# Kernel tuning notes

Measured on AMD Instinct MI355X. Metric: run time of the kernel, lower is better.

The kernel has to match this reference:

```python
import jax, jax.numpy as jnp
import numpy as np

N = 50000      # nodes
E = 1600000    # edges (avg degree 32)
C_IN = 128
C_H = 128
C_OUT = 10
G = 512        # number of graphs in the batch


def setup_inputs() -> dict:
    key = jax.random.key(0)
    ks = jax.random.split(key, 16)
    x = jax.random.normal(ks[0], (N, C_IN), dtype=jnp.float32)
    edge_index = jax.random.randint(ks[1], (2, E), 0, N, dtype=jnp.int64)
    batch = jnp.sort(jax.random.randint(ks[2], (N,), 0, G, dtype=jnp.int64))

    def lin(k, fan_in, fan_out):
        lim = 1.0 / np.sqrt(fan_in)
        return jax.random.uniform(k, (fan_in, fan_out), jnp.float32, -lim, lim)

    return {
        "x": x, "edge_index": edge_index, "batch": batch,
        # conv1: c_in -> c_hidden
        "Wr1": lin(ks[3], C_IN, C_H), "br1": jnp.zeros((C_H,), jnp.float32),
        "Wo1": lin(ks[4], C_IN, C_H),
        # conv2: c_hidden -> 2*c_hidden
        "Wr2": lin(ks[5], C_H, 2 * C_H), "br2": jnp.zeros((2 * C_H,), jnp.float32),
        "Wo2": lin(ks[6], C_H, 2 * C_H),
        # conv3: 2*c_hidden -> c_hidden
        "Wr3": lin(ks[7], 2 * C_H, C_H), "br3": jnp.zeros((C_H,), jnp.float32),
        "Wo3": lin(ks[8], 2 * C_H, C_H),
        # head
        "W1": lin(ks[9], C_H, 4 * C_OUT), "b1": jnp.zeros((4 * C_OUT,), jnp.float32),
        "W2": lin(ks[10], 4 * C_OUT, C_OUT), "b2": jnp.zeros((C_OUT,), jnp.float32),
    }


def _graph_conv(x, src, dst, Wr, br, Wo):
    # PyG GraphConv: lin_rel(sum_{j in N(i)} x_j) + lin_root(x_i)
    agg = jax.ops.segment_sum(x[src], dst, num_segments=N)  # [N, F_in]
    return agg @ Wr + br + x @ Wo


def reference(x, edge_index, batch, Wr1, br1, Wo1, Wr2, br2, Wo2,
              Wr3, br3, Wo3, W1, b1, W2, b2):
    src, dst = edge_index[0], edge_index[1]
    h = jax.nn.relu(_graph_conv(x, src, dst, Wr1, br1, Wo1))
    h = jax.nn.relu(_graph_conv(h, src, dst, Wr2, br2, Wo2))
    h = _graph_conv(h, src, dst, Wr3, br3, Wo3)
    # global mean pool over graphs
    sums = jax.ops.segment_sum(h, batch, num_segments=G)            # [G, C_H]
    cnts = jax.ops.segment_sum(jnp.ones((N,), h.dtype), batch, num_segments=G)
    pooled = sums / jnp.maximum(cnts, 1.0)[:, None]
    # dropout is identity in eval mode
    out = pooled @ W1 + b1
    out = out @ W2 + b2
    return out
```

## Files before the change

kernel.cpp:

```cpp
#include <hip/hip_runtime.h>
#include <hip/hip_bf16.h>
#include <cstddef>

#define NN 50000
#define EE 1600000
#define GG 512
#define NB 196
#define BSTRIDE 16384
#define BCAP 10240
#define XBLKS 6250
#define SCBLKS 782

typedef unsigned int u32;
typedef unsigned short u16;
typedef __attribute__((ext_vector_type(8))) short frag_ab;
typedef __attribute__((ext_vector_type(4))) float frag_cd;

__device__ __forceinline__ void gl_lds16(const void* g, void* l) {
    __builtin_amdgcn_global_load_lds(
        (const __attribute__((address_space(1))) u32*)g,
        (__attribute__((address_space(3))) u32*)l, 16, 0, 0);
}
__device__ __forceinline__ float b2f_lo(u32 v) { return __uint_as_float(v << 16); }
__device__ __forceinline__ float b2f_hi(u32 v) { return __uint_as_float(v & 0xffff0000u); }
__device__ __forceinline__ float b2f(u32 v, int odd) { return odd ? b2f_hi(v) : b2f_lo(v); }
__device__ __forceinline__ u16 f2b(float x) {
    __hip_bfloat16 h = __float2bfloat16(x);
    return *(u16*)&h;
}
__device__ __forceinline__ u32 pack2(float lo, float hi) {
    return ((u32)f2b(hi) << 16) | f2b(lo);
}
__device__ __forceinline__ void acc2(float2& a, u32 v) {
    a.x += b2f_lo(v);
    a.y += b2f_hi(v);
}


__global__ __launch_bounds__(256) void bscatter_prep_kernel(
    const int* __restrict__ ei, int* __restrict__ bcnt, u32* __restrict__ pairs,
    const float* __restrict__ x, u16* __restrict__ ax,
    const float* __restrict__ Wr1, const float* __restrict__ Wo1,
    const float* __restrict__ Wr2, const float* __restrict__ Wo2,
    const float* __restrict__ Wr3, const float* __restrict__ Wo3,
    const float* __restrict__ br3,
    u16* __restrict__ BT1, u16* __restrict__ BT2, u16* __restrict__ BT3,
    float* __restrict__ bias3) {
    __shared__ int lcnt[NB];
    __shared__ int lbase[NB];
    __shared__ unsigned short lpos[2048];
    int bid = blockIdx.x, t = threadIdx.x;
    if (bid < SCBLKS) {
        int e0 = bid * 2048;
        u32 pk[8];
        int bk[8];
        for (int i = t; i < NB; i += 256) lcnt[i] = 0;
        __syncthreads();
#pragma unroll
        for (int i = 0; i < 8; ++i) {
            int e = e0 + i * 256 + t;
            if (e < EE) {
                int dst = ei[EE + e], src = ei[e];
                int b = dst >> 8;
                bk[i] = b;
                pk[i] = ((u32)src << 8) | (u32)(dst & 255);
                lpos[i * 256 + t] = (unsigned short)atomicAdd(&lcnt[b], 1);
            } else bk[i] = -1;
        }
        __syncthreads();
        for (int i = t; i < NB; i += 256) lbase[i] = atomicAdd(&bcnt[i], lcnt[i]);
        __syncthreads();
#pragma unroll
        for (int i = 0; i < 8; ++i) {
            if (bk[i] >= 0) {
                int pos = lbase[bk[i]] + (int)lpos[i * 256 + t];
                pairs[(size_t)bk[i] * BSTRIDE + pos] = pk[i];
            }
        }
    } else if (bid < SCBLKS + XBLKS) {
        int idx = (bid - SCBLKS) * 256 + t;
        int row = idx >> 5, q = idx & 31;
        float4 v = *(const float4*)(x + (size_t)row * 128 + q * 4);
        *(u32*)(ax + (size_t)row * 256 + 128 + q * 4) = pack2(v.x, v.y);
        *(u32*)(ax + (size_t)row * 256 + 128 + q * 4 + 2) = pack2(v.z, v.w);
    } else {
        int m = bid - SCBLKS - XBLKS;
        int k = t;
        BT2[m * 256 + k] = f2b(k < 128 ? Wr2[k * 256 + m] : Wo2[(k - 128) * 256 + m]);
        BT3[m * 256 + k] = f2b(m < 128 ? Wr3[k * 128 + m] : Wo3[k * 128 + (m - 128)]);
        if (m < 128)
            BT1[m * 256 + k] = f2b(k < 128 ? Wr1[k * 128 + m] : Wo1[(k - 128) * 128 + m]);
        if (k == 0) bias3[m] = (m < 128) ? 0.f : br3[m - 128];
    }
}


__global__ __launch_bounds__(512) void bfill_kernel(const u32* __restrict__ pairs,
                                                    const int* __restrict__ bcnt,
                                                    int* __restrict__ ofs,
                                                    u16* __restrict__ srcl) {
    __shared__ int sc[256];
    __shared__ int cnts[256];
    __shared__ int lcnt[256];
    __shared__ int lcur[256];
    __shared__ int lbuf[BCAP];
    int b = blockIdx.x, t = threadIdx.x;
    if (t < 256) {
        int c = (t < NB) ? bcnt[t] : 0;
        cnts[t] = c;
        sc[t] = c;
        lcnt[t] = 0;
    }
    __syncthreads();
    for (int off = 1; off < 256; off <<= 1) {
        int v = (t >= off && t < 256) ? sc[t - off] : 0;
        __syncthreads();
        if (t < 256) sc[t] += v;
        __syncthreads();
    }
    int base = sc[b] - cnts[b];
    int span = cnts[b];
    const u32* pp = pairs + (size_t)b * BSTRIDE;
    for (int j = t; j < span; j += 512) atomicAdd(&lcnt[pp[j] & 255u], 1);
    __syncthreads();
    int nc = 0;
    if (t < 256) {
        nc = lcnt[t];
        sc[t] = nc;
    }
    __syncthreads();
    for (int off = 1; off < 256; off <<= 1) {
        int v = (t >= off && t < 256) ? sc[t - off] : 0;
        __syncthreads();
        if (t < 256) sc[t] += v;
        __syncthreads();
    }
    if (t < 256) {
        int excl = sc[t] - nc;
        int node = b * 256 + t;
        if (node < NN) ofs[node] = base + excl;
        lcur[t] = excl;
    }
    if (b == 0 && t == 256) ofs[NN] = EE;
    __syncthreads();
    for (int j = t; j < span; j += 512) {
        u32 p = pp[j];
        int pos = atomicAdd(&lcur[p & 255u], 1);
        int src = (int)(p >> 8);
        if (pos < BCAP) lbuf[pos] = src;
        else srcl[base + pos] = (u16)src;
    }
    __syncthreads();
    int lim = span < BCAP ? span : BCAP;
    for (int j = t; j < lim; j += 512) srcl[base + j] = (u16)lbuf[j];
}


__global__ __launch_bounds__(256) void pull_bf_kernel(const u32* __restrict__ Xu,
                                                      const int* __restrict__ ofs,
                                                      const u16* __restrict__ srcl,
                                                      u32* __restrict__ outu) {
    int node = (blockIdx.x * 256 + threadIdx.x) >> 6;
    int lane = threadIdx.x & 63;
    int q = lane >> 4, l = lane & 15;
    int lo = ofs[node], hi = ofs[node + 1];
    float2 a0 = {0.f, 0.f}, a1 = {0.f, 0.f}, a2 = {0.f, 0.f}, a3 = {0.f, 0.f};
    int j = lo;
    for (; j + 15 < hi; j += 16) {
        int s0 = srcl[j + q], s1 = srcl[j + 4 + q];
        int s2 = srcl[j + 8 + q], s3 = srcl[j + 12 + q];
        uint4 v0 = *(const uint4*)(Xu + (size_t)s0 * 128 + l * 4);
        uint4 v1 = *(const uint4*)(Xu + (size_t)s1 * 128 + l * 4);
        uint4 v2 = *(const uint4*)(Xu + (size_t)s2 * 128 + l * 4);
        uint4 v3 = *(const uint4*)(Xu + (size_t)s3 * 128 + l * 4);
        acc2(a0, v0.x); acc2(a1, v0.y); acc2(a2, v0.z); acc2(a3, v0.w);
        acc2(a0, v1.x); acc2(a1, v1.y); acc2(a2, v1.z); acc2(a3, v1.w);
        acc2(a0, v2.x); acc2(a1, v2.y); acc2(a2, v2.z); acc2(a3, v2.w);
        acc2(a0, v3.x); acc2(a1, v3.y); acc2(a2, v3.z); acc2(a3, v3.w);
    }
    for (; j + 3 < hi; j += 4) {
        int s = srcl[j + q];
        uint4 v = *(const uint4*)(Xu + (size_t)s * 128 + l * 4);
        acc2(a0, v.x); acc2(a1, v.y); acc2(a2, v.z); acc2(a3, v.w);
    }
    if (j + q < hi) {
        int s = srcl[j + q];
        uint4 v = *(const uint4*)(Xu + (size_t)s * 128 + l * 4);
        acc2(a0, v.x); acc2(a1, v.y); acc2(a2, v.z); acc2(a3, v.w);
    }
    float acc[8] = {a0.x, a0.y, a1.x, a1.y, a2.x, a2.y, a3.x, a3.y};
#pragma unroll
    for (int i = 0; i < 8; ++i) {
        acc[i] += __shfl_xor(acc[i], 16, 64);
        acc[i] += __shfl_xor(acc[i], 32, 64);
    }
    if (q == 0) {
        uint4 r;
        r.x = pack2(acc[0], acc[1]);
        r.y = pack2(acc[2], acc[3]);
        r.z = pack2(acc[4], acc[5]);
        r.w = pack2(acc[6], acc[7]);
        *(uint4*)(outu + (size_t)node * 128 + l * 4) = r;
    }
}

__global__ __launch_bounds__(256) void pull3_kernel(const u32* __restrict__ Tu,
                                                    const int* __restrict__ ofs,
                                                    const u16* __restrict__ srcl,
                                                    u32* __restrict__ h3u) {
    int node = (blockIdx.x * 256 + threadIdx.x) >> 6;
    int lane = threadIdx.x & 63;
    int q = lane >> 4, l = lane & 15;
    int lo = ofs[node], hi = ofs[node + 1];
    float2 a0 = {0.f, 0.f}, a1 = {0.f, 0.f}, a2 = {0.f, 0.f}, a3 = {0.f, 0.f};
    int j = lo;
    for (; j + 15 < hi; j += 16) {
        int s0 = srcl[j + q], s1 = srcl[j + 4 + q];
        int s2 = srcl[j + 8 + q], s3 = srcl[j + 12 + q];
        uint4 v0 = *(const uint4*)(Tu + (size_t)s0 * 128 + l * 4);
        uint4 v1 = *(const uint4*)(Tu + (size_t)s1 * 128 + l * 4);
        uint4 v2 = *(const uint4*)(Tu + (size_t)s2 * 128 + l * 4);
        uint4 v3 = *(const uint4*)(Tu + (size_t)s3 * 128 + l * 4);
        acc2(a0, v0.x); acc2(a1, v0.y); acc2(a2, v0.z); acc2(a3, v0.w);
        acc2(a0, v1.x); acc2(a1, v1.y); acc2(a2, v1.z); acc2(a3, v1.w);
        acc2(a0, v2.x); acc2(a1, v2.y); acc2(a2, v2.z); acc2(a3, v2.w);
        acc2(a0, v3.x); acc2(a1, v3.y); acc2(a2, v3.z); acc2(a3, v3.w);
    }
    for (; j + 3 < hi; j += 4) {
        int s = srcl[j + q];
        uint4 v = *(const uint4*)(Tu + (size_t)s * 128 + l * 4);
        acc2(a0, v.x); acc2(a1, v.y); acc2(a2, v.z); acc2(a3, v.w);
    }
    if (j + q < hi) {
        int s = srcl[j + q];
        uint4 v = *(const uint4*)(Tu + (size_t)s * 128 + l * 4);
        acc2(a0, v.x); acc2(a1, v.y); acc2(a2, v.z); acc2(a3, v.w);
    }
    float acc[8] = {a0.x, a0.y, a1.x, a1.y, a2.x, a2.y, a3.x, a3.y};
#pragma unroll
    for (int i = 0; i < 8; ++i) {
        acc[i] += __shfl_xor(acc[i], 16, 64);
        acc[i] += __shfl_xor(acc[i], 32, 64);
    }
    if (q == 0) {
        uint4 o = *(const uint4*)(Tu + (size_t)node * 128 + 64 + l * 4);
        acc[0] += b2f_lo(o.x); acc[1] += b2f_hi(o.x);
        acc[2] += b2f_lo(o.y); acc[3] += b2f_hi(o.y);
        acc[4] += b2f_lo(o.z); acc[5] += b2f_hi(o.z);
        acc[6] += b2f_lo(o.w); acc[7] += b2f_hi(o.w);
        uint4 r;
        r.x = pack2(acc[0], acc[1]);
        r.y = pack2(acc[2], acc[3]);
        r.z = pack2(acc[4], acc[5]);
        r.w = pack2(acc[6], acc[7]);
        *(uint4*)(h3u + (size_t)node * 64 + l * 4) = r;
    }
}


__global__ __launch_bounds__(256, 2) void gemm_bf_kernel(
    const u16* __restrict__ A, const u16* __restrict__ BT,
    const float* __restrict__ bias, u16* __restrict__ C,
    int ldc, int coloff, int relu) {
    __shared__ alignas(16) u16 As[128 * 32];
    __shared__ alignas(16) u16 Bs[128 * 32];
    const int t = threadIdx.x;
    const int lane = t & 63, wid = t >> 6;
    const int quad = lane >> 4, l16 = lane & 15;
    const int wm = wid >> 1, wn = wid & 1;
    const int row0 = blockIdx.y * 128, c0 = blockIdx.x * 128;

    frag_cd acc[4][4];
#pragma unroll
    for (int i = 0; i < 4; ++i)
#pragma unroll
        for (int j = 0; j < 4; ++j) acc[i][j] = (frag_cd)0.f;

    const int ca = t, cb = t + 256;
    const int ra = ca >> 2, oa = (ca & 3) * 8;
    const int rb = cb >> 2, ob = (cb & 3) * 8;
    const int garow = min(row0 + ra, NN - 1);
    const int gbrow = min(row0 + rb, NN - 1);
    const size_t gA1 = (size_t)garow * 256 + oa;
    const size_t gA2 = (size_t)gbrow * 256 + ob;
    const size_t gB1 = (size_t)(c0 + ra) * 256 + oa;
    const size_t gB2 = (size_t)(c0 + rb) * 256 + ob;

    for (int kk = 0; kk < 256; kk += 32) {
        __syncthreads();
        gl_lds16(A + gA1 + kk, &As[ca * 8]);
        gl_lds16(A + gA2 + kk, &As[cb * 8]);
        gl_lds16(BT + gB1 + kk, &Bs[ca * 8]);
        gl_lds16(BT + gB2 + kk, &Bs[cb * 8]);
        __syncthreads();

        frag_ab a[4], b[4];
#pragma unroll
        for (int mt = 0; mt < 4; ++mt)
            a[mt] = *(const frag_ab*)&As[(wm * 64 + mt * 16 + l16) * 32 + quad * 8];
#pragma unroll
        for (int nt = 0; nt < 4; ++nt)
            b[nt] = *(const frag_ab*)&Bs[(wn * 64 + nt * 16 + l16) * 32 + quad * 8];
#pragma unroll
        for (int mt = 0; mt < 4; ++mt)
#pragma unroll
            for (int nt = 0; nt < 4; ++nt)
                acc[mt][nt] = __builtin_amdgcn_mfma_f32_16x16x32_bf16(
                    a[mt], b[nt], acc[mt][nt], 0, 0, 0);
    }

#pragma unroll
    for (int nt = 0; nt < 4; ++nt) {
        int col = c0 + wn * 64 + nt * 16 + l16;
        float bv = bias[col];
#pragma unroll
        for (int mt = 0; mt < 4; ++mt) {
#pragma unroll
            for (int r = 0; r < 4; ++r) {
                int row = row0 + wm * 64 + mt * 16 + quad * 4 + r;
                if (row < NN) {
                    float v = acc[mt][nt][r] + bv;
                    if (relu) v = fmaxf(v, 0.f);
                    C[(size_t)row * ldc + coloff + col] = f2b(v);
                }
            }
        }
    }
}


__device__ inline int lower_bound_i(const int* a, int n, int v) {
    int lo = 0, hi = n;
    while (lo < hi) {
        int m = (lo + hi) >> 1;
        if (a[m] < v) lo = m + 1; else hi = m;
    }
    return lo;
}

__global__ __launch_bounds__(256) void pool_head_kernel(const u32* __restrict__ h3u,
                                                        const int* __restrict__ batch,
                                                        const float* __restrict__ W1,
                                                        const float* __restrict__ b1,
                                                        const float* __restrict__ W2,
                                                        const float* __restrict__ b2,
                                                        float* __restrict__ out) {
    __shared__ float ps[256];
    __shared__ float p[128];
    __shared__ float hid[40];
    int g = blockIdx.x, t = threadIdx.x;
    int c = t & 127, half = t >> 7;
    int w = c >> 1, odd = c & 1;
    int lo = lower_bound_i(batch, NN, g);
    int hi = lower_bound_i(batch, NN, g + 1);
    float s = 0.f;
    int i = lo + half;
    for (; i + 6 < hi; i += 8) {
        u32 v0 = h3u[(size_t)i * 64 + w];
        u32 v1 = h3u[(size_t)(i + 2) * 64 + w];
        u32 v2 = h3u[(size_t)(i + 4) * 64 + w];
        u32 v3 = h3u[(size_t)(i + 6) * 64 + w];
        s += (b2f(v0, odd) + b2f(v1, odd)) + (b2f(v2, odd) + b2f(v3, odd));
    }
    for (; i < hi; i += 2) s += b2f(h3u[(size_t)i * 64 + w], odd);
    ps[t] = s;
    __syncthreads();
    if (half == 0) p[c] = (ps[c] + ps[c + 128]) / fmaxf((float)(hi - lo), 1.f);
    __syncthreads();
    if (t < 40) {
        float v = b1[t];
        for (int k = 0; k < 128; ++k) v += p[k] * W1[k * 40 + t];
        hid[t] = v;
    }
    __syncthreads();
    if (t < 10) {
        float v = b2[t];
        for (int j = 0; j < 40; ++j) v += hid[j] * W2[j * 10 + t];
        out[g * 10 + t] = v;
    }
}


extern "C" void kernel_launch(void* const* d_in, const int* in_sizes, int n_in,
                              void* d_out, int out_size, void* d_ws, size_t ws_size,
                              hipStream_t stream) {
    const float* x   = (const float*)d_in[0];
    const int* ei    = (const int*)d_in[1];
    const int* batch = (const int*)d_in[2];
    const float* Wr1 = (const float*)d_in[3];
    const float* br1 = (const float*)d_in[4];
    const float* Wo1 = (const float*)d_in[5];
    const float* Wr2 = (const float*)d_in[6];
    const float* br2 = (const float*)d_in[7];
    const float* Wo2 = (const float*)d_in[8];
    const float* Wr3 = (const float*)d_in[9];
    const float* br3 = (const float*)d_in[10];
    const float* Wo3 = (const float*)d_in[11];
    const float* W1  = (const float*)d_in[12];
    const float* b1  = (const float*)d_in[13];
    const float* W2  = (const float*)d_in[14];
    const float* b2  = (const float*)d_in[15];
    float* out = (float*)d_out;

    char* ws = (char*)d_ws;
    size_t off = 0;
    auto alloc = [&](size_t bytes) {
        void* p = ws + off;
        off += (bytes + 255) & ~(size_t)255;
        return p;
    };
    int* ofs      = (int*)alloc((NN + 1) * sizeof(int));
    int* bcnt     = (int*)alloc(256 * sizeof(int));
    u16* srcl     = (u16*)alloc((size_t)EE * 2);
    u16* ax       = (u16*)alloc((size_t)NN * 256 * 2);
    u16* ah1      = (u16*)alloc((size_t)NN * 256 * 2);
    u16* h2       = (u16*)alloc((size_t)NN * 256 * 2);
    u16* t3o3     = (u16*)alloc((size_t)NN * 256 * 2);
    u16* h3       = (u16*)alloc((size_t)NN * 128 * 2);
    u16* BT1      = (u16*)alloc(128 * 256 * 2);
    u16* BT2      = (u16*)alloc(256 * 256 * 2);
    u16* BT3      = (u16*)alloc(256 * 256 * 2);
    float* bias3  = (float*)alloc(256 * sizeof(float));
    u32* pairs = (u32*)h2;

    hipMemsetAsync(bcnt, 0, 256 * sizeof(int), stream);

    bscatter_prep_kernel<<<SCBLKS + XBLKS + 256, 256, 0, stream>>>(
        ei, bcnt, pairs, x, ax, Wr1, Wo1, Wr2, Wo2, Wr3, Wo3, br3,
        BT1, BT2, BT3, bias3);
    bfill_kernel<<<NB, 512, 0, stream>>>(pairs, bcnt, ofs, srcl);

    pull_bf_kernel<<<NN * 64 / 256, 256, 0, stream>>>((const u32*)ax + 64, ofs, srcl, (u32*)ax);
    gemm_bf_kernel<<<dim3(1, 391), 256, 0, stream>>>(ax, BT1, br1, ah1, 256, 128, 1);
    pull_bf_kernel<<<NN * 64 / 256, 256, 0, stream>>>((const u32*)ah1 + 64, ofs, srcl, (u32*)ah1);
    gemm_bf_kernel<<<dim3(2, 391), 256, 0, stream>>>(ah1, BT2, br2, h2, 256, 0, 1);
    gemm_bf_kernel<<<dim3(2, 391), 256, 0, stream>>>(h2, BT3, bias3, t3o3, 256, 0, 0);
    pull3_kernel<<<NN * 64 / 256, 256, 0, stream>>>((const u32*)t3o3, ofs, srcl, (u32*)h3);

    pool_head_kernel<<<GG, 256, 0, stream>>>((const u32*)h3, batch, W1, b1, W2, b2, out);
}
```

Baseline: 360.8 us.

## Split gathered features into 32-column slabs for cache-friendly gather passes

Stores the gathered node features in four column-sliced slabs (32 bf16 per row, 64 bytes) instead of 256-wide interleaved rows. Each gather kernel now runs four passes over the grid, one per slab, so each pass's working set is a quarter of the feature matrix and may stay resident in L2/MALL. The GEMM gains modes to read the split layout and write sliced or row-major outputs. The cost is more lanes per edge, extra shuffle reductions, four times more index reads, and less efficient 64-byte gathers.

Result: slower. 472.9 us (+31.1%).

```diff
diff --git a/kernel.cpp b/kernel.cpp
--- a/kernel.cpp
+++ b/kernel.cpp
@@ -37,9 +37,10 @@
 }
 
 
+
 __global__ __launch_bounds__(256) void bscatter_prep_kernel(
     const int* __restrict__ ei, int* __restrict__ bcnt, u32* __restrict__ pairs,
-    const float* __restrict__ x, u16* __restrict__ ax,
+    const float* __restrict__ x, u32* __restrict__ xslu,
     const float* __restrict__ Wr1, const float* __restrict__ Wo1,
     const float* __restrict__ Wr2, const float* __restrict__ Wo2,
     const float* __restrict__ Wr3, const float* __restrict__ Wo3,
@@ -81,8 +82,12 @@
         int idx = (bid - SCBLKS) * 256 + t;
         int row = idx >> 5, q = idx & 31;
         float4 v = *(const float4*)(x + (size_t)row * 128 + q * 4);
-        *(u32*)(ax + (size_t)row * 256 + 128 + q * 4) = pack2(v.x, v.y);
-        *(u32*)(ax + (size_t)row * 256 + 128 + q * 4 + 2) = pack2(v.z, v.w);
+        int s = q >> 3;
+        u32* dst = xslu + (((size_t)(s * NN + row)) << 4) + ((q & 7) << 1);
+        uint2 w;
+        w.x = pack2(v.x, v.y);
+        w.y = pack2(v.z, v.w);
+        *(uint2*)dst = w;
     } else {
         int m = bid - SCBLKS - XBLKS;
         int k = t;
@@ -156,41 +161,40 @@
 }
 
 
-__global__ __launch_bounds__(256) void pull_bf_kernel(const u32* __restrict__ Xu,
+__global__ __launch_bounds__(256) void pull_sl_kernel(const u32* __restrict__ Xsl,
                                                       const int* __restrict__ ofs,
                                                       const u16* __restrict__ srcl,
-                                                      u32* __restrict__ outu) {
-    int node = (blockIdx.x * 256 + threadIdx.x) >> 6;
+                                                      u32* __restrict__ aggu) {
+    int node = blockIdx.x * 4 + (threadIdx.x >> 6);
+    int p = blockIdx.y;
     int lane = threadIdx.x & 63;
-    int q = lane >> 4, l = lane & 15;
+    int q = lane >> 2, l = lane & 3;
+    const u32* base = Xsl + ((size_t)p * NN << 4);
     int lo = ofs[node], hi = ofs[node + 1];
     float2 a0 = {0.f, 0.f}, a1 = {0.f, 0.f}, a2 = {0.f, 0.f}, a3 = {0.f, 0.f};
     int j = lo;
-    for (; j + 15 < hi; j += 16) {
-        int s0 = srcl[j + q], s1 = srcl[j + 4 + q];
-        int s2 = srcl[j + 8 + q], s3 = srcl[j + 12 + q];
-        uint4 v0 = *(const uint4*)(Xu + (size_t)s0 * 128 + l * 4);
-        uint4 v1 = *(const uint4*)(Xu + (size_t)s1 * 128 + l * 4);
-        uint4 v2 = *(const uint4*)(Xu + (size_t)s2 * 128 + l * 4);
-        uint4 v3 = *(const uint4*)(Xu + (size_t)s3 * 128 + l * 4);
+    for (; j + 31 < hi; j += 32) {
+        int s0 = srcl[j + q], s1 = srcl[j + 16 + q];
+        uint4 v0 = *(const uint4*)(base + ((size_t)s0 << 4) + l * 4);
+        uint4 v1 = *(const uint4*)(base + ((size_t)s1 << 4) + l * 4);
         acc2(a0, v0.x); acc2(a1, v0.y); acc2(a2, v0.z); acc2(a3, v0.w);
         acc2(a0, v1.x); acc2(a1, v1.y); acc2(a2, v1.z); acc2(a3, v1.w);
-        acc2(a0, v2.x); acc2(a1, v2.y); acc2(a2, v2.z); acc2(a3, v2.w);
-        acc2(a0, v3.x); acc2(a1, v3.y); acc2(a2, v3.z); acc2(a3, v3.w);
-    }
-    for (; j + 3 < hi; j += 4) {
+    }
+    for (; j + 15 < hi; j += 16) {
         int s = srcl[j + q];
-        uint4 v = *(const uint4*)(Xu + (size_t)s * 128 + l * 4);
+        uint4 v = *(const uint4*)(base + ((size_t)s << 4) + l * 4);
         acc2(a0, v.x); acc2(a1, v.y); acc2(a2, v.z); acc2(a3, v.w);
     }
     if (j + q < hi) {
         int s = srcl[j + q];
-        uint4 v = *(const uint4*)(Xu + (size_t)s * 128 + l * 4);
+        uint4 v = *(const uint4*)(base + ((size_t)s << 4) + l * 4);
         acc2(a0, v.x); acc2(a1, v.y); acc2(a2, v.z); acc2(a3, v.w);
     }
     float acc[8] = {a0.x, a0.y, a1.x, a1.y, a2.x, a2.y, a3.x, a3.y};
 #pragma unroll
     for (int i = 0; i < 8; ++i) {
+        acc[i] += __shfl_xor(acc[i], 4, 64);
+        acc[i] += __shfl_xor(acc[i], 8, 64);
         acc[i] += __shfl_xor(acc[i], 16, 64);
         acc[i] += __shfl_xor(acc[i], 32, 64);
     }
@@ -200,50 +204,50 @@
         r.y = pack2(acc[2], acc[3]);
         r.z = pack2(acc[4], acc[5]);
         r.w = pack2(acc[6], acc[7]);
-        *(uint4*)(outu + (size_t)node * 128 + l * 4) = r;
-    }
-}
-
-__global__ __launch_bounds__(256) void pull3_kernel(const u32* __restrict__ Tu,
-                                                    const int* __restrict__ ofs,
-                                                    const u16* __restrict__ srcl,
-                                                    u32* __restrict__ h3u) {
-    int node = (blockIdx.x * 256 + threadIdx.x) >> 6;
+        *(uint4*)(aggu + (size_t)node * 64 + p * 16 + l * 4) = r;
+    }
+}
+
+__global__ __launch_bounds__(256) void pull3_sl_kernel(const u32* __restrict__ Tsl,
+                                                       const u32* __restrict__ o3u,
+                                                       const int* __restrict__ ofs,
+                                                       const u16* __restrict__ srcl,
+                                                       u32* __restrict__ h3u) {
+    int node = blockIdx.x * 4 + (threadIdx.x >> 6);
+    int p = blockIdx.y;
     int lane = threadIdx.x & 63;
-    int q = lane >> 4, l = lane & 15;
+    int q = lane >> 2, l = lane & 3;
+    const u32* base = Tsl + ((size_t)p * NN << 4);
     int lo = ofs[node], hi = ofs[node + 1];
     float2 a0 = {0.f, 0.f}, a1 = {0.f, 0.f}, a2 = {0.f, 0.f}, a3 = {0.f, 0.f};
     int j = lo;
-    for (; j + 15 < hi; j += 16) {
-        int s0 = srcl[j + q], s1 = srcl[j + 4 + q];
-        int s2 = srcl[j + 8 + q], s3 = srcl[j + 12 + q];
-        uint4 v0 = *(const uint4*)(Tu + (size_t)s0 * 128 + l * 4);
-        uint4 v1 = *(const uint4*)(Tu + (size_t)s1 * 128 + l * 4);
-        uint4 v2 = *(const uint4*)(Tu + (size_t)s2 * 128 + l * 4);
-        uint4 v3 = *(const uint4*)(Tu + (size_t)s3 * 128 + l * 4);
+    for (; j + 31 < hi; j += 32) {
+        int s0 = srcl[j + q], s1 = srcl[j + 16 + q];
+        uint4 v0 = *(const uint4*)(base + ((size_t)s0 << 4) + l * 4);
+        uint4 v1 = *(const uint4*)(base + ((size_t)s1 << 4) + l * 4);
         acc2(a0, v0.x); acc2(a1, v0.y); acc2(a2, v0.z); acc2(a3, v0.w);
         acc2(a0, v1.x); acc2(a1, v1.y); acc2(a2, v1.z); acc2(a3, v1.w);
-        acc2(a0, v2.x); acc2(a1, v2.y); acc2(a2, v2.z); acc2(a3, v2.w);
-        acc2(a0, v3.x); acc2(a1, v3.y); acc2(a2, v3.z); acc2(a3, v3.w);
-    }
-    for (; j + 3 < hi; j += 4) {
+    }
+    for (; j + 15 < hi; j += 16) {
         int s = srcl[j + q];
-        uint4 v = *(const uint4*)(Tu + (size_t)s * 128 + l * 4);
+        uint4 v = *(const uint4*)(base + ((size_t)s << 4) + l * 4);
         acc2(a0, v.x); acc2(a1, v.y); acc2(a2, v.z); acc2(a3, v.w);
     }
     if (j + q < hi) {
         int s = srcl[j + q];
-        uint4 v = *(const uint4*)(Tu + (size_t)s * 128 + l * 4);
+        uint4 v = *(const uint4*)(base + ((size_t)s << 4) + l * 4);
         acc2(a0, v.x); acc2(a1, v.y); acc2(a2, v.z); acc2(a3, v.w);
     }
     float acc[8] = {a0.x, a0.y, a1.x, a1.y, a2.x, a2.y, a3.x, a3.y};
 #pragma unroll
     for (int i = 0; i < 8; ++i) {
+        acc[i] += __shfl_xor(acc[i], 4, 64);
+        acc[i] += __shfl_xor(acc[i], 8, 64);
         acc[i] += __shfl_xor(acc[i], 16, 64);
         acc[i] += __shfl_xor(acc[i], 32, 64);
     }
     if (q == 0) {
-        uint4 o = *(const uint4*)(Tu + (size_t)node * 128 + 64 + l * 4);
+        uint4 o = *(const uint4*)(o3u + (size_t)node * 64 + p * 16 + l * 4);
         acc[0] += b2f_lo(o.x); acc[1] += b2f_hi(o.x);
         acc[2] += b2f_lo(o.y); acc[3] += b2f_hi(o.y);
         acc[4] += b2f_lo(o.z); acc[5] += b2f_hi(o.z);
@@ -253,15 +257,16 @@
         r.y = pack2(acc[2], acc[3]);
         r.z = pack2(acc[4], acc[5]);
         r.w = pack2(acc[6], acc[7]);
-        *(uint4*)(h3u + (size_t)node * 64 + l * 4) = r;
+        *(uint4*)(h3u + (size_t)node * 64 + p * 16 + l * 4) = r;
     }
 }
 
 
 __global__ __launch_bounds__(256, 2) void gemm_bf_kernel(
-    const u16* __restrict__ A, const u16* __restrict__ BT,
-    const float* __restrict__ bias, u16* __restrict__ C,
-    int ldc, int coloff, int relu) {
+    const u16* __restrict__ A0, const u16* __restrict__ A1,
+    const u16* __restrict__ BT, const float* __restrict__ bias,
+    u16* __restrict__ C0, u16* __restrict__ C1,
+    int amode, int cmode, int relu) {
     __shared__ alignas(16) u16 As[128 * 32];
     __shared__ alignas(16) u16 Bs[128 * 32];
     const int t = threadIdx.x;
@@ -281,17 +286,25 @@
     const int rb = cb >> 2, ob = (cb & 3) * 8;
     const int garow = min(row0 + ra, NN - 1);
     const int gbrow = min(row0 + rb, NN - 1);
-    const size_t gA1 = (size_t)garow * 256 + oa;
-    const size_t gA2 = (size_t)gbrow * 256 + ob;
-    const size_t gB1 = (size_t)(c0 + ra) * 256 + oa;
-    const size_t gB2 = (size_t)(c0 + rb) * 256 + ob;
 
     for (int kk = 0; kk < 256; kk += 32) {
-        __syncthreads();
-        gl_lds16(A + gA1 + kk, &As[ca * 8]);
-        gl_lds16(A + gA2 + kk, &As[cb * 8]);
-        gl_lds16(BT + gB1 + kk, &Bs[ca * 8]);
-        gl_lds16(BT + gB2 + kk, &Bs[cb * 8]);
+        const u16 *pa, *pb;
+        if (amode) {
+            pa = A0 + (size_t)garow * 256 + kk + oa;
+            pb = A0 + (size_t)gbrow * 256 + kk + ob;
+        } else if (kk < 128) {
+            pa = A0 + (size_t)garow * 128 + kk + oa;
+            pb = A0 + (size_t)gbrow * 128 + kk + ob;
+        } else {
+            int s = (kk >> 5) - 4;
+            pa = A1 + (((size_t)(s * NN + garow)) << 5) + oa;
+            pb = A1 + (((size_t)(s * NN + gbrow)) << 5) + ob;
+        }
+        __syncthreads();
+        gl_lds16(pa, &As[ca * 8]);
+        gl_lds16(pb, &As[cb * 8]);
+        gl_lds16(BT + (size_t)(c0 + ra) * 256 + kk + oa, &Bs[ca * 8]);
+        gl_lds16(BT + (size_t)(c0 + rb) * 256 + kk + ob, &Bs[cb * 8]);
         __syncthreads();
 
         frag_ab a[4], b[4];
@@ -311,7 +324,8 @@
 
 #pragma unroll
     for (int nt = 0; nt < 4; ++nt) {
-        int col = c0 + wn * 64 + nt * 16 + l16;
+        int col128 = wn * 64 + nt * 16 + l16;
+        int col = c0 + col128;
         float bv = bias[col];
 #pragma unroll
         for (int mt = 0; mt < 4; ++mt) {
@@ -321,7 +335,17 @@
                 if (row < NN) {
                     float v = acc[mt][nt][r] + bv;
                     if (relu) v = fmaxf(v, 0.f);
-                    C[(size_t)row * ldc + coloff + col] = f2b(v);
+                    u16 hv = f2b(v);
+                    if (cmode == 0) {
+                        C0[(((size_t)((col128 >> 5) * NN + row)) << 5) + (col128 & 31)] = hv;
+                    } else if (cmode == 1) {
+                        C0[(size_t)row * 256 + col] = hv;
+                    } else {
+                        if (col < 128)
+                            C0[(((size_t)((col >> 5) * NN + row)) << 5) + (col & 31)] = hv;
+                        else
+                            C1[(size_t)row * 128 + (col - 128)] = hv;
+                    }
                 }
             }
         }
@@ -412,10 +436,13 @@
     int* ofs      = (int*)alloc((NN + 1) * sizeof(int));
     int* bcnt     = (int*)alloc(256 * sizeof(int));
     u16* srcl     = (u16*)alloc((size_t)EE * 2);
-    u16* ax       = (u16*)alloc((size_t)NN * 256 * 2);
-    u16* ah1      = (u16*)alloc((size_t)NN * 256 * 2);
+    u16* xsl      = (u16*)alloc((size_t)NN * 128 * 2);
+    u16* agg1     = (u16*)alloc((size_t)NN * 128 * 2);
+    u16* h1sl     = (u16*)alloc((size_t)NN * 128 * 2);
+    u16* agg2     = (u16*)alloc((size_t)NN * 128 * 2);
     u16* h2       = (u16*)alloc((size_t)NN * 256 * 2);
-    u16* t3o3     = (u16*)alloc((size_t)NN * 256 * 2);
+    u16* t3sl     = (u16*)alloc((size_t)NN * 128 * 2);
+    u16* o3       = (u16*)alloc((size_t)NN * 128 * 2);
     u16* h3       = (u16*)alloc((size_t)NN * 128 * 2);
     u16* BT1      = (u16*)alloc(128 * 256 * 2);
     u16* BT2      = (u16*)alloc(256 * 256 * 2);
@@ -426,16 +453,22 @@
     hipMemsetAsync(bcnt, 0, 256 * sizeof(int), stream);
 
     bscatter_prep_kernel<<<SCBLKS + XBLKS + 256, 256, 0, stream>>>(
-        ei, bcnt, pairs, x, ax, Wr1, Wo1, Wr2, Wo2, Wr3, Wo3, br3,
+        ei, bcnt, pairs, x, (u32*)xsl, Wr1, Wo1, Wr2, Wo2, Wr3, Wo3, br3,
         BT1, BT2, BT3, bias3);
     bfill_kernel<<<NB, 512, 0, stream>>>(pairs, bcnt, ofs, srcl);
 
-    pull_bf_kernel<<<NN * 64 / 256, 256, 0, stream>>>((const u32*)ax + 64, ofs, srcl, (u32*)ax);
-    gemm_bf_kernel<<<dim3(1, 391), 256, 0, stream>>>(ax, BT1, br1, ah1, 256, 128, 1);
-    pull_bf_kernel<<<NN * 64 / 256, 256, 0, stream>>>((const u32*)ah1 + 64, ofs, srcl, (u32*)ah1);
-    gemm_bf_kernel<<<dim3(2, 391), 256, 0, stream>>>(ah1, BT2, br2, h2, 256, 0, 1);
-    gemm_bf_kernel<<<dim3(2, 391), 256, 0, stream>>>(h2, BT3, bias3, t3o3, 256, 0, 0);
-    pull3_kernel<<<NN * 64 / 256, 256, 0, stream>>>((const u32*)t3o3, ofs, srcl, (u32*)h3);
+    pull_sl_kernel<<<dim3(NN / 4, 4), 256, 0, stream>>>(
+        (const u32*)xsl, ofs, srcl, (u32*)agg1);
+    gemm_bf_kernel<<<dim3(1, 391), 256, 0, stream>>>(
+        agg1, xsl, BT1, br1, h1sl, nullptr, 0, 0, 1);
+    pull_sl_kernel<<<dim3(NN / 4, 4), 256, 0, stream>>>(
+        (const u32*)h1sl, ofs, srcl, (u32*)agg2);
+    gemm_bf_kernel<<<dim3(2, 391), 256, 0, stream>>>(
+        agg2, h1sl, BT2, br2, h2, nullptr, 0, 1, 1);
+    gemm_bf_kernel<<<dim3(2, 391), 256, 0, stream>>>(
+        h2, nullptr, BT3, bias3, t3sl, o3, 1, 2, 0);
+    pull3_sl_kernel<<<dim3(NN / 4, 4), 256, 0, stream>>>(
+        (const u32*)t3sl, (const u32*)o3, ofs, srcl, (u32*)h3);
 
     pool_head_kernel<<<GG, 256, 0, stream>>>((const u32*)h3, batch, W1, b1, W2, b2, out);
 }
```

## Fuse conv2 and conv3 GEMMs keeping hidden tile in LDS

Applied to the files above, without the earlier changes.

Replaces the two back-to-back GEMM launches (conv2 with ReLU, then conv3's combined weights) with one kernel that computes a 128-row tile of h2 into a 64 KB swizzled LDS buffer and feeds it straight into the second GEMM. This removes the global write and re-read of the N×256 bf16 h2 intermediate and one launch. In exchange, each block uses about 80 KB of LDS, which limits occupancy. The grid also shrinks to 391 blocks covering all 256 columns, and the staging loop has no double buffering.

New measurement: 352.5 us. 2.3% less time.

```diff
diff --git a/kernel.cpp b/kernel.cpp
--- a/kernel.cpp
+++ b/kernel.cpp
@@ -35,6 +35,7 @@
     a.x += b2f_lo(v);
     a.y += b2f_hi(v);
 }
+
 
 
 __global__ __launch_bounds__(256) void bscatter_prep_kernel(
@@ -322,6 +323,124 @@
                     float v = acc[mt][nt][r] + bv;
                     if (relu) v = fmaxf(v, 0.f);
                     C[(size_t)row * ldc + coloff + col] = f2b(v);
+                }
+            }
+        }
+    }
+}
+
+
+__global__ __launch_bounds__(256, 2) void gemm23_kernel(
+    const u16* __restrict__ A, const u16* __restrict__ BT2,
+    const float* __restrict__ br2, const u16* __restrict__ BT3,
+    const float* __restrict__ bias3, u16* __restrict__ C) {
+    __shared__ alignas(16) u16 As[128 * 32];
+    __shared__ alignas(16) u16 Bs[128 * 32];
+    __shared__ alignas(16) u16 Hs[128 * 256];
+    const int t = threadIdx.x;
+    const int lane = t & 63, wid = t >> 6;
+    const int quad = lane >> 4, l16 = lane & 15;
+    const int wm = wid >> 1, wn = wid & 1;
+    const int row0 = blockIdx.x * 128;
+
+    const int ca = t, cb = t + 256;
+    const int ra = ca >> 2, oa = (ca & 3) * 8;
+    const int rb = cb >> 2, ob = (cb & 3) * 8;
+    const int garow = min(row0 + ra, NN - 1);
+    const int gbrow = min(row0 + rb, NN - 1);
+    const size_t gA1 = (size_t)garow * 256 + oa;
+    const size_t gA2 = (size_t)gbrow * 256 + ob;
+
+    for (int nb = 0; nb < 2; ++nb) {
+        const int c0 = nb * 128;
+        frag_cd acc[4][4];
+#pragma unroll
+        for (int i = 0; i < 4; ++i)
+#pragma unroll
+            for (int j = 0; j < 4; ++j) acc[i][j] = (frag_cd)0.f;
+
+        for (int kk = 0; kk < 256; kk += 32) {
+            __syncthreads();
+            gl_lds16(A + gA1 + kk, &As[ca * 8]);
+            gl_lds16(A + gA2 + kk, &As[cb * 8]);
+            gl_lds16(BT2 + (size_t)(c0 + ra) * 256 + kk + oa, &Bs[ca * 8]);
+            gl_lds16(BT2 + (size_t)(c0 + rb) * 256 + kk + ob, &Bs[cb * 8]);
+            __syncthreads();
+
+            frag_ab a[4], b[4];
+#pragma unroll
+            for (int mt = 0; mt < 4; ++mt)
+                a[mt] = *(const frag_ab*)&As[(wm * 64 + mt * 16 + l16) * 32 + quad * 8];
+#pragma unroll
+            for (int nt = 0; nt < 4; ++nt)
+                b[nt] = *(const frag_ab*)&Bs[(wn * 64 + nt * 16 + l16) * 32 + quad * 8];
+#pragma unroll
+            for (int mt = 0; mt < 4; ++mt)
+#pragma unroll
+                for (int nt = 0; nt < 4; ++nt)
+                    acc[mt][nt] = __builtin_amdgcn_mfma_f32_16x16x32_bf16(
+                        a[mt], b[nt], acc[mt][nt], 0, 0, 0);
+        }
+#pragma unroll
+        for (int nt = 0; nt < 4; ++nt) {
+            int col = c0 + wn * 64 + nt * 16 + l16;
+            float bv = br2[col];
+#pragma unroll
+            for (int mt = 0; mt < 4; ++mt) {
+#pragma unroll
+                for (int r = 0; r < 4; ++r) {
+                    int lr = wm * 64 + mt * 16 + quad * 4 + r;
+                    float v = fmaxf(acc[mt][nt][r] + bv, 0.f);
+                    Hs[(lr * 256 + col) ^ ((lr & 7) << 3)] = f2b(v);
+                }
+            }
+        }
+    }
+    __syncthreads();
+
+    for (int nb = 0; nb < 2; ++nb) {
+        const int c0 = nb * 128;
+        frag_cd acc[4][4];
+#pragma unroll
+        for (int i = 0; i < 4; ++i)
+#pragma unroll
+            for (int j = 0; j < 4; ++j) acc[i][j] = (frag_cd)0.f;
+
+        for (int kk = 0; kk < 256; kk += 32) {
+            __syncthreads();
+            gl_lds16(BT3 + (size_t)(c0 + ra) * 256 + kk + oa, &Bs[ca * 8]);
+            gl_lds16(BT3 + (size_t)(c0 + rb) * 256 + kk + ob, &Bs[cb * 8]);
+            __syncthreads();
+
+            frag_ab a[4], b[4];
+#pragma unroll
+            for (int mt = 0; mt < 4; ++mt) {
+                int lr = wm * 64 + mt * 16 + l16;
+                a[mt] = *(const frag_ab*)&Hs[(lr * 256 + kk + quad * 8) ^ ((lr & 7) << 3)];
+            }
+#pragma unroll
+            for (int nt = 0; nt < 4; ++nt)
+                b[nt] = *(const frag_ab*)&Bs[(wn * 64 + nt * 16 + l16) * 32 + quad * 8];
+#pragma unroll
+            for (int mt = 0; mt < 4; ++mt)
+#pragma unroll
+                for (int nt = 0; nt < 4; ++nt)
+                    acc[mt][nt] = __builtin_amdgcn_mfma_f32_16x16x32_bf16(
+                        a[mt], b[nt], acc[mt][nt], 0, 0, 0);
+        }
+#pragma unroll
+        for (int nt = 0; nt < 4; ++nt) {
+            int col = c0 + wn * 64 + nt * 16 + l16;
+            float bv = bias3[col];
+#pragma unroll
+            for (int mt = 0; mt < 4; ++mt) {
+#pragma unroll
+                for (int r = 0; r < 4; ++r) {
+                    int row = row0 + wm * 64 + mt * 16 + quad * 4 + r;
+                    if (row < NN) {
+                        float v = acc[mt][nt][r] + bv;
+                        C[(size_t)row * 256 + col] = f2b(v);
+                    }
                 }
             }
         }
@@ -414,14 +533,13 @@
     u16* srcl     = (u16*)alloc((size_t)EE * 2);
     u16* ax       = (u16*)alloc((size_t)NN * 256 * 2);
     u16* ah1      = (u16*)alloc((size_t)NN * 256 * 2);
-    u16* h2       = (u16*)alloc((size_t)NN * 256 * 2);
     u16* t3o3     = (u16*)alloc((size_t)NN * 256 * 2);
     u16* h3       = (u16*)alloc((size_t)NN * 128 * 2);
     u16* BT1      = (u16*)alloc(128 * 256 * 2);
     u16* BT2      = (u16*)alloc(256 * 256 * 2);
     u16* BT3      = (u16*)alloc(256 * 256 * 2);
     float* bias3  = (float*)alloc(256 * sizeof(float));
-    u32* pairs = (u32*)h2;
+    u32* pairs = (u32*)t3o3;
 
     hipMemsetAsync(bcnt, 0, 256 * sizeof(int), stream);
 
@@ -433,8 +551,7 @@
     pull_bf_kernel<<<NN * 64 / 256, 256, 0, stream>>>((const u32*)ax + 64, ofs, srcl, (u32*)ax);
     gemm_bf_kernel<<<dim3(1, 391), 256, 0, stream>>>(ax, BT1, br1, ah1, 256, 128, 1);
     pull_bf_kernel<<<NN * 64 / 256, 256, 0, stream>>>((const u32*)ah1 + 64, ofs, srcl, (u32*)ah1);
-    gemm_bf_kernel<<<dim3(2, 391), 256, 0, stream>>>(ah1, BT2, br2, h2, 256, 0, 1);
-    gemm_bf_kernel<<<dim3(2, 391), 256, 0, stream>>>(h2, BT3, bias3, t3o3, 256, 0, 0);
+    gemm23_kernel<<<391, 256, 0, stream>>>(ah1, BT2, br2, BT3, bias3, t3o3);
     pull3_kernel<<<NN * 64 / 256, 256, 0, stream>>>((const u32*)t3o3, ofs, srcl, (u32*)h3);
 
     pool_head_kernel<<<GG, 256, 0, stream>>>((const u32*)h3, batch, W1, b1, W2, b2, out);
```
